# Optimization experiments

Measured on AMD Instinct MI355X. Metric: run time of the kernel, lower is better.

Reference implementation:

```python
import jax, jax.numpy as jnp
import numpy as np

D = 256          # input_dim (node embedding dim)
ATT_TIMES = 2
ATT_NUM = 2
DIN = D * ATT_NUM  # NTN input dim = 512
F = 16           # feature_map_dim


def setup_inputs() -> dict:
    key = jax.random.key(0)
    ks = jax.random.split(key, 10)
    x1 = jax.random.normal(ks[0], (120000, D), dtype=jnp.float32)
    x2 = jax.random.normal(ks[1], (100000, D), dtype=jnp.float32)
    # attention weight (glorot)
    W0 = jax.random.normal(ks[2], (D, D), dtype=jnp.float32) * (2.0 / (D + D)) ** 0.5
    # NTN params
    V = jax.random.normal(ks[3], (F, 2 * DIN), dtype=jnp.float32) * (2.0 / (F + 2 * DIN)) ** 0.5
    W = jax.random.normal(ks[4], (F, DIN, DIN), dtype=jnp.float32) * (2.0 / (DIN + DIN)) ** 0.5
    b = jax.random.normal(ks[5], (F,), dtype=jnp.float32)
    # projection MLP 16->8->4->2->1, torch Linear weights are (out, in)
    P0 = jax.random.normal(ks[6], (8, 16), dtype=jnp.float32) * (2.0 / (8 + 16)) ** 0.5
    P1 = jax.random.normal(ks[7], (4, 8), dtype=jnp.float32) * (2.0 / (4 + 8)) ** 0.5
    P2 = jax.random.normal(ks[8], (2, 4), dtype=jnp.float32) * (2.0 / (2 + 4)) ** 0.5
    P3 = jax.random.normal(ks[9], (1, 2), dtype=jnp.float32) * (2.0 / (1 + 2)) ** 0.5
    return {"x1": x1, "x2": x2, "W0": W0, "V": V, "W": W, "b": b,
            "P0": P0, "P1": P1, "P2": P2, "P3": P3}


def _attention(x, W0):
    # x: (N, D) -> (1, D*ATT_NUM) graph embedding.
    outs = []
    for _ in range(ATT_NUM):  # 'dot' style: same params each head (eye W), kept for faithfulness
        cur = x
        out = None
        for _ in range(ATT_TIMES):
            temp = jnp.mean(cur, axis=0, keepdims=True)          # (1, D)
            h_avg = jnp.tanh(temp @ W0)                          # att_weight=True
            att = jax.nn.sigmoid(cur @ h_avg.T)                  # (N, 1), W=eye in 'dot' style
            out = att.T @ cur                                    # (1, D)
            cur = cur * att
        outs.append(out)
    return jnp.concatenate(outs, axis=1)                         # (1, DIN)


def _ntn(g1, g2, V, W, b):
    # g1, g2: (1, DIN). Fused bilinear over all F feature maps.
    concat = jnp.concatenate([g1, g2], axis=1)                   # (1, 2*DIN)
    v_term = concat @ V.T                                        # (1, F)
    w_term = jnp.einsum('nd,fde,me->nf', g1, W, g2)              # (1, F)
    return jax.nn.sigmoid(v_term + w_term + b)                   # inneract = sigmoid


def reference(x1, x2, W0, V, W, b, P0, P1, P2, P3):
    g1 = _attention(x1, W0)
    g2 = _attention(x2, W0)
    x = _ntn(g1, g2, V, W, b)                                    # (1, F), branch 'an'
    for P in (P0, P1, P2, P3):                                   # Linear(no bias) + Sigmoid
        x = jax.nn.sigmoid(x @ P.T)
    return x                                                     # (1, 1)
```

## Files before the change

kernel.cpp:

```cpp
#include <hip/hip_runtime.h>
#include <math.h>

#define DD 256
#define REPS 8

#define OFF_SUMREP 0
#define OFF_H1P    4096
#define OFF_S1REP  4608
#define OFF_H2P    8704
#define OFF_OREP   9216
#define OFF_WTREP  13824
#define WS_FLOATS  13952
#define MIRROR_OFF_BYTES 65536

typedef float    f32x4 __attribute__((ext_vector_type(4)));
typedef float    f32x8 __attribute__((ext_vector_type(8)));
typedef _Float16 f16x4 __attribute__((ext_vector_type(4)));
typedef _Float16 f16x8 __attribute__((ext_vector_type(8)));

__device__ __forceinline__ float sigmoidf_(float x) { return 1.0f / (1.0f + __expf(-x)); }

__device__ __forceinline__ f32x8 ld8(const f16x8* p, size_t i) {
    return __builtin_convertvector(p[i], f32x8);
}
__device__ __forceinline__ f32x8 ld8(const f32x8* p, size_t i) { return p[i]; }

__device__ __forceinline__ float dot8(f32x8 a, f32x8 b) {
    f32x8 m = a * b;
    return ((m[0] + m[4]) + (m[1] + m[5])) + ((m[2] + m[6]) + (m[3] + m[7]));
}

__global__ void k_zero(float* __restrict__ ws) {
    int i = blockIdx.x * 256 + threadIdx.x;
    if (i < WS_FLOATS) ws[i] = 0.0f;
}

__device__ __forceinline__ void block_reduce_atomic4(f32x4 acc, int t, float* dst_base) {
    __shared__ f32x4 lds[256];
    lds[t] = acc;
    __syncthreads();
    if (t < 64) {
        f32x4 s = lds[t] + lds[t + 64] + lds[t + 128] + lds[t + 192];
        float* dst = dst_base + t * 4;
        atomicAdd(dst + 0, s.x); atomicAdd(dst + 1, s.y);
        atomicAdd(dst + 2, s.z); atomicAdd(dst + 3, s.w);
    }
}

__device__ __forceinline__ void block_reduce_atomic8(f32x8 acc, int t, float* dst_base) {
    __shared__ f32x8 lds8[256];
    lds8[t] = acc;
    __syncthreads();
    const float* lf = (const float*)lds8;
    float s = 0.f;
#pragma unroll
    for (int slot = 0; slot < 8; slot++) s += lf[slot * 256 + t];
    atomicAdd(dst_base + t, s);
}

template<bool WM>
__global__ void k_mean_t(const f32x4* __restrict__ x1, const f32x4* __restrict__ x2,
                         f16x4* __restrict__ m1, f16x4* __restrict__ m2,
                         int N1, int N2, float* __restrict__ ws) {
    int b = blockIdx.x, t = threadIdx.x;
    int inp = (b < 512) ? 0 : 1;
    int bl = inp ? (b - 512) : b;
    const f32x4* x = inp ? x2 : x1;
    f16x4* mm = inp ? m2 : m1;
    int N = inp ? N2 : N1;
    int col4 = t & 63, rg = t >> 6;
    f32x4 acc = {0.f, 0.f, 0.f, 0.f};
    for (int r = bl * 4 + rg; r < N; r += 2048) {
        size_t i0 = (size_t)r * 64 + col4;
        f32x4 v = x[i0];
        if (WM) mm[i0] = __builtin_convertvector(v, f16x4);
        acc += v;
    }
    block_reduce_atomic4(acc, t, ws + OFF_SUMREP + inp * (REPS * 256) + (bl & (REPS - 1)) * 256);
}

__global__ void k_hpart(const float* __restrict__ W0, float* __restrict__ ws,
                        int srcOff, int dstOff, int N1, int N2) {
    int inp = blockIdx.x >> 4, g = blockIdx.x & 15;
    int t = threadIdx.x;
    __shared__ float temp[16];
    if (t < 16) {
        const float* src = ws + srcOff + inp * (REPS * 256) + g * 16 + t;
        float s = 0.f;
#pragma unroll
        for (int r = 0; r < REPS; r++) s += src[r * 256];
        temp[t] = s * (1.0f / (float)(inp ? N2 : N1));
    }
    __syncthreads();
    float p = 0.f;
#pragma unroll
    for (int j = 0; j < 16; j++) p += temp[j] * W0[(g * 16 + j) * 256 + t];
    atomicAdd(ws + dstOff + inp * 256 + t, p);
}

template<typename T>
__global__ void k_att1_t(const T* __restrict__ b1, const T* __restrict__ b2,
                         int N1, int N2, float* __restrict__ ws) {
    int b = blockIdx.x, t = threadIdx.x;
    int inp = (b < 512) ? 0 : 1;
    int bl = inp ? (b - 512) : b;
    const T* x = inp ? b2 : b1;
    int N = inp ? N2 : N1;
    int lane = t & 63, w = t >> 6;
    int half = lane >> 5, l32 = lane & 31;
    f32x8 h1;
#pragma unroll
    for (int j = 0; j < 8; j++) h1[j] = tanhf(ws[OFF_H1P + inp * 256 + l32 * 8 + j]);
    f32x8 acc = {0.f, 0.f, 0.f, 0.f, 0.f, 0.f, 0.f, 0.f};
    int wid = bl * 4 + w;
    int base = wid * 2;
    for (; base + 1 < N; base += 4096) {
        int row = base + half;
        f32x8 v = ld8(x, (size_t)row * 32 + l32);
        float d = dot8(v, h1);
#pragma unroll
        for (int off = 16; off; off >>= 1) d += __shfl_xor(d, off, 64);
        acc += sigmoidf_(d) * v;
    }
    if (base < N && half == 0) {
        f32x8 v = ld8(x, (size_t)base * 32 + l32);
        float d = dot8(v, h1);
#pragma unroll
        for (int off = 16; off; off >>= 1) d += __shfl_xor(d, off, 64);
        acc += sigmoidf_(d) * v;
    }
    block_reduce_atomic8(acc, t, ws + OFF_S1REP + inp * (REPS * 256) + (bl & (REPS - 1)) * 256);
}

template<typename T>
__global__ void k_att2_t(const T* __restrict__ b1, const T* __restrict__ b2,
                         int N1, int N2, float* __restrict__ ws) {
    int b = blockIdx.x, t = threadIdx.x;
    int inp = (b < 512) ? 0 : 1;
    int bl = inp ? (b - 512) : b;
    const T* x = inp ? b2 : b1;
    int N = inp ? N2 : N1;
    int lane = t & 63, w = t >> 6;
    int half = lane >> 5, l32 = lane & 31;
    f32x8 h1, h2;
#pragma unroll
    for (int j = 0; j < 8; j++) {
        h1[j] = tanhf(ws[OFF_H1P + inp * 256 + l32 * 8 + j]);
        h2[j] = tanhf(ws[OFF_H2P + inp * 256 + l32 * 8 + j]);
    }
    f32x8 acc = {0.f, 0.f, 0.f, 0.f, 0.f, 0.f, 0.f, 0.f};
    int wid = bl * 4 + w;
    int base = wid * 2;
    for (; base + 1 < N; base += 4096) {
        int row = base + half;
        f32x8 v = ld8(x, (size_t)row * 32 + l32);
        float d = dot8(v, h1), e = dot8(v, h2);
#pragma unroll
        for (int off = 16; off; off >>= 1) {
            d += __shfl_xor(d, off, 64); e += __shfl_xor(e, off, 64);
        }
        float a1 = sigmoidf_(d);
        acc += (a1 * sigmoidf_(a1 * e)) * v;
    }
    if (base < N && half == 0) {
        f32x8 v = ld8(x, (size_t)base * 32 + l32);
        float d = dot8(v, h1), e = dot8(v, h2);
#pragma unroll
        for (int off = 16; off; off >>= 1) {
            d += __shfl_xor(d, off, 64); e += __shfl_xor(e, off, 64);
        }
        float a1 = sigmoidf_(d);
        acc += (a1 * sigmoidf_(a1 * e)) * v;
    }
    block_reduce_atomic8(acc, t, ws + OFF_OREP + inp * (REPS * 256) + (bl & (REPS - 1)) * 256);
}

__global__ void __launch_bounds__(256, 4)
k_ntn(const float* __restrict__ W, float* __restrict__ ws) {
    __shared__ __align__(16) float o_l[512];
    int b = blockIdx.x, t = threadIdx.x;
    {
        float s0 = 0.f, s1 = 0.f;
#pragma unroll
        for (int r2 = 0; r2 < REPS; r2++) {
            s0 += ws[OFF_OREP + r2 * 256 + t];
            s1 += ws[OFF_OREP + REPS * 256 + r2 * 256 + t];
        }
        o_l[t] = s0; o_l[256 + t] = s1;
    }
    __syncthreads();
    int lane = t & 63, w = t >> 6;
    f32x4 o2f = ((const f32x4*)(o_l + 256))[lane];
    int g = b * 4 + w;
    const f32x4* W4 = (const f32x4*)W;
    float wt[4];
    int fidx[4];
#pragma unroll
    for (int u = 0; u < 4; u++) {
        int row = g + u * 2048;
        const f32x4* q = W4 + (size_t)row * 128 + lane;
        f32x4 m = (q[0] + q[64]) * o2f;
        float p = (m.x + m.y) + (m.z + m.w);
#pragma unroll
        for (int off = 32; off; off >>= 1) p += __shfl_xor(p, off, 64);
        wt[u] = o_l[row & 255] * p;
        fidx[u] = row >> 9;
    }
    if (lane == 0) {
        float* dst = ws + OFF_WTREP + (b & (REPS - 1)) * 16;
#pragma unroll
        for (int u = 0; u < 4; u++) atomicAdd(dst + fidx[u], wt[u]);
    }
}

__global__ void k_final(const float* __restrict__ V, const float* __restrict__ bb,
                        const float* __restrict__ P0, const float* __restrict__ P1,
                        const float* __restrict__ P2, const float* __restrict__ P3,
                        float* __restrict__ ws, float* __restrict__ out) {
    int t = threadIdx.x;
    __shared__ float o_l[512];
    {
        float s0 = 0.f, s1 = 0.f;
#pragma unroll
        for (int r2 = 0; r2 < REPS; r2++) {
            s0 += ws[OFF_OREP + r2 * 256 + t];
            s1 += ws[OFF_OREP + REPS * 256 + r2 * 256 + t];
        }
        o_l[t] = s0; o_l[256 + t] = s1;
    }
    __syncthreads();
    int f = t >> 4, j = t & 15;
    float p = 0.f;
    for (int k = j; k < 1024; k += 16) {
        float cv = (k < 512) ? o_l[k & 255] : o_l[256 + (k & 255)];
        p += cv * V[f * 1024 + k];
    }
    __shared__ float red[256];
    __shared__ float sv[16];
    red[t] = p;
    __syncthreads();
    if (t < 16) {
        float v = 0.f;
#pragma unroll
        for (int q = 0; q < 16; q++) v += red[t * 16 + q];
        float wt = 0.f;
#pragma unroll
        for (int r = 0; r < REPS; r++) wt += ws[OFF_WTREP + r * 16 + t];
        sv[t] = sigmoidf_(v + wt + bb[t]);
    }
    __syncthreads();
    if (t == 0) {
        float y0[8], y1[4], y2[2];
#pragma unroll
        for (int i = 0; i < 8; i++) {
            float s = 0.f;
            for (int k = 0; k < 16; k++) s += P0[i * 16 + k] * sv[k];
            y0[i] = sigmoidf_(s);
        }
#pragma unroll
        for (int i = 0; i < 4; i++) {
            float s = 0.f;
            for (int k = 0; k < 8; k++) s += P1[i * 8 + k] * y0[k];
            y1[i] = sigmoidf_(s);
        }
#pragma unroll
        for (int i = 0; i < 2; i++) {
            float s = 0.f;
            for (int k = 0; k < 4; k++) s += P2[i * 4 + k] * y1[k];
            y2[i] = sigmoidf_(s);
        }
        out[0] = sigmoidf_(P3[0] * y2[0] + P3[1] * y2[1]);
    }
}

extern "C" void kernel_launch(void* const* d_in, const int* in_sizes, int n_in,
                              void* d_out, int out_size, void* d_ws, size_t ws_size,
                              hipStream_t stream) {
    const float* x1 = (const float*)d_in[0];
    const float* x2 = (const float*)d_in[1];
    const float* W0 = (const float*)d_in[2];
    const float* V  = (const float*)d_in[3];
    const float* W  = (const float*)d_in[4];
    const float* b  = (const float*)d_in[5];
    const float* P0 = (const float*)d_in[6];
    const float* P1 = (const float*)d_in[7];
    const float* P2 = (const float*)d_in[8];
    const float* P3 = (const float*)d_in[9];
    float* ws  = (float*)d_ws;
    float* out = (float*)d_out;
    int N1 = in_sizes[0] / DD;
    int N2 = in_sizes[1] / DD;

    const f32x4* x1v = (const f32x4*)x1;
    const f32x4* x2v = (const f32x4*)x2;
    f16x4* m1 = (f16x4*)((char*)d_ws + MIRROR_OFF_BYTES);
    f16x4* m2 = m1 + (size_t)N1 * 64;
    size_t need = (size_t)MIRROR_OFF_BYTES + ((size_t)N1 + N2) * DD * sizeof(_Float16);
    bool use_mirror = ws_size >= need;

    k_zero <<<55, 256, 0, stream>>>(ws);
    if (use_mirror) {
        k_mean_t<true>  <<<1024, 256, 0, stream>>>(x1v, x2v, m1, m2, N1, N2, ws);
        k_hpart         <<<32,   256, 0, stream>>>(W0, ws, OFF_SUMREP, OFF_H1P, N1, N2);
        k_att1_t<f16x8> <<<1024, 256, 0, stream>>>((const f16x8*)m1, (const f16x8*)m2, N1, N2, ws);
        k_hpart         <<<32,   256, 0, stream>>>(W0, ws, OFF_S1REP, OFF_H2P, N1, N2);
        k_att2_t<f16x8> <<<1024, 256, 0, stream>>>((const f16x8*)m1, (const f16x8*)m2, N1, N2, ws);
    } else {
        k_mean_t<false> <<<1024, 256, 0, stream>>>(x1v, x2v, nullptr, nullptr, N1, N2, ws);
        k_hpart         <<<32,   256, 0, stream>>>(W0, ws, OFF_SUMREP, OFF_H1P, N1, N2);
        k_att1_t<f32x8> <<<1024, 256, 0, stream>>>((const f32x8*)x1, (const f32x8*)x2, N1, N2, ws);
        k_hpart         <<<32,   256, 0, stream>>>(W0, ws, OFF_S1REP, OFF_H2P, N1, N2);
        k_att2_t<f32x8> <<<1024, 256, 0, stream>>>((const f32x8*)x1, (const f32x8*)x2, N1, N2, ws);
    }
    k_ntn  <<<512, 256, 0, stream>>>(W, ws);
    k_final<<<1,   256, 0, stream>>>(V, b, P0, P1, P2, P3, ws, out);
}
```

Baseline: 402.2 us.

## Drop fp16 mirror; stream fp32 inputs with wider grids and unrolled column sum

Removes the fp16 mirror copy of x1/x2 written during the mean pass. Both attention passes now read the original fp32 inputs directly, with the attention grids doubled to 2048 blocks. The column sum becomes a separate per-input kernel with four independent accumulators over a flat strided index. This drops the mirror write traffic but doubles the bytes each attention pass reads, so the net effect depends on whether the fp32 data stays in cache (the inputs total about 225 MB).

```diff
diff --git a/kernel.cpp b/kernel.cpp
--- a/kernel.cpp
+++ b/kernel.cpp
@@ -11,19 +11,11 @@
 #define OFF_OREP   9216
 #define OFF_WTREP  13824
 #define WS_FLOATS  13952
-#define MIRROR_OFF_BYTES 65536
 
 typedef float    f32x4 __attribute__((ext_vector_type(4)));
 typedef float    f32x8 __attribute__((ext_vector_type(8)));
-typedef _Float16 f16x4 __attribute__((ext_vector_type(4)));
-typedef _Float16 f16x8 __attribute__((ext_vector_type(8)));
 
 __device__ __forceinline__ float sigmoidf_(float x) { return 1.0f / (1.0f + __expf(-x)); }
-
-__device__ __forceinline__ f32x8 ld8(const f16x8* p, size_t i) {
-    return __builtin_convertvector(p[i], f32x8);
-}
-__device__ __forceinline__ f32x8 ld8(const f32x8* p, size_t i) { return p[i]; }
 
 __device__ __forceinline__ float dot8(f32x8 a, f32x8 b) {
     f32x8 m = a * b;
@@ -58,25 +50,23 @@
     atomicAdd(dst_base + t, s);
 }
 
-template<bool WM>
-__global__ void k_mean_t(const f32x4* __restrict__ x1, const f32x4* __restrict__ x2,
-                         f16x4* __restrict__ m1, f16x4* __restrict__ m2,
-                         int N1, int N2, float* __restrict__ ws) {
-    int b = blockIdx.x, t = threadIdx.x;
-    int inp = (b < 512) ? 0 : 1;
-    int bl = inp ? (b - 512) : b;
-    const f32x4* x = inp ? x2 : x1;
-    f16x4* mm = inp ? m2 : m1;
-    int N = inp ? N2 : N1;
-    int col4 = t & 63, rg = t >> 6;
-    f32x4 acc = {0.f, 0.f, 0.f, 0.f};
-    for (int r = bl * 4 + rg; r < N; r += 2048) {
-        size_t i0 = (size_t)r * 64 + col4;
-        f32x4 v = x[i0];
-        if (WM) mm[i0] = __builtin_convertvector(v, f16x4);
-        acc += v;
-    }
-    block_reduce_atomic4(acc, t, ws + OFF_SUMREP + inp * (REPS * 256) + (bl & (REPS - 1)) * 256);
+__global__ void k_colsum(const f32x4* __restrict__ x, int N, int inp,
+                         float* __restrict__ ws) {
+    int t = threadIdx.x;
+    const size_t STR = 1024 * 256;
+    size_t total = (size_t)N * 64;
+    size_t i = (size_t)blockIdx.x * 256 + t;
+    f32x4 a0 = {0.f,0.f,0.f,0.f}, a1 = a0, a2 = a0, a3 = a0;
+    for (; i + 3 * STR < total; i += 4 * STR) {
+        a0 += x[i];
+        a1 += x[i + STR];
+        a2 += x[i + 2 * STR];
+        a3 += x[i + 3 * STR];
+    }
+    for (; i < total; i += STR) a0 += x[i];
+    f32x4 acc = (a0 + a1) + (a2 + a3);
+    block_reduce_atomic4(acc, t,
+        ws + OFF_SUMREP + inp * (REPS * 256) + (blockIdx.x & (REPS - 1)) * 256);
 }
 
 __global__ void k_hpart(const float* __restrict__ W0, float* __restrict__ ws,
@@ -98,13 +88,12 @@
     atomicAdd(ws + dstOff + inp * 256 + t, p);
 }
 
-template<typename T>
-__global__ void k_att1_t(const T* __restrict__ b1, const T* __restrict__ b2,
-                         int N1, int N2, float* __restrict__ ws) {
+__global__ void k_att1(const f32x8* __restrict__ b1, const f32x8* __restrict__ b2,
+                       int N1, int N2, float* __restrict__ ws) {
     int b = blockIdx.x, t = threadIdx.x;
-    int inp = (b < 512) ? 0 : 1;
-    int bl = inp ? (b - 512) : b;
-    const T* x = inp ? b2 : b1;
+    int inp = (b < 1024) ? 0 : 1;
+    int bl = inp ? (b - 1024) : b;
+    const f32x8* x = inp ? b2 : b1;
     int N = inp ? N2 : N1;
     int lane = t & 63, w = t >> 6;
     int half = lane >> 5, l32 = lane & 31;
@@ -114,16 +103,16 @@
     f32x8 acc = {0.f, 0.f, 0.f, 0.f, 0.f, 0.f, 0.f, 0.f};
     int wid = bl * 4 + w;
     int base = wid * 2;
-    for (; base + 1 < N; base += 4096) {
+    for (; base + 1 < N; base += 8192) {
         int row = base + half;
-        f32x8 v = ld8(x, (size_t)row * 32 + l32);
+        f32x8 v = x[(size_t)row * 32 + l32];
         float d = dot8(v, h1);
 #pragma unroll
         for (int off = 16; off; off >>= 1) d += __shfl_xor(d, off, 64);
         acc += sigmoidf_(d) * v;
     }
     if (base < N && half == 0) {
-        f32x8 v = ld8(x, (size_t)base * 32 + l32);
+        f32x8 v = x[(size_t)base * 32 + l32];
         float d = dot8(v, h1);
 #pragma unroll
         for (int off = 16; off; off >>= 1) d += __shfl_xor(d, off, 64);
@@ -132,13 +121,12 @@
     block_reduce_atomic8(acc, t, ws + OFF_S1REP + inp * (REPS * 256) + (bl & (REPS - 1)) * 256);
 }
 
-template<typename T>
-__global__ void k_att2_t(const T* __restrict__ b1, const T* __restrict__ b2,
-                         int N1, int N2, float* __restrict__ ws) {
+__global__ void k_att2(const f32x8* __restrict__ b1, const f32x8* __restrict__ b2,
+                       int N1, int N2, float* __restrict__ ws) {
     int b = blockIdx.x, t = threadIdx.x;
-    int inp = (b < 512) ? 0 : 1;
-    int bl = inp ? (b - 512) : b;
-    const T* x = inp ? b2 : b1;
+    int inp = (b < 1024) ? 0 : 1;
+    int bl = inp ? (b - 1024) : b;
+    const f32x8* x = inp ? b2 : b1;
     int N = inp ? N2 : N1;
     int lane = t & 63, w = t >> 6;
     int half = lane >> 5, l32 = lane & 31;
@@ -151,9 +139,9 @@
     f32x8 acc = {0.f, 0.f, 0.f, 0.f, 0.f, 0.f, 0.f, 0.f};
     int wid = bl * 4 + w;
     int base = wid * 2;
-    for (; base + 1 < N; base += 4096) {
+    for (; base + 1 < N; base += 8192) {
         int row = base + half;
-        f32x8 v = ld8(x, (size_t)row * 32 + l32);
+        f32x8 v = x[(size_t)row * 32 + l32];
         float d = dot8(v, h1), e = dot8(v, h2);
 #pragma unroll
         for (int off = 16; off; off >>= 1) {
@@ -163,7 +151,7 @@
         acc += (a1 * sigmoidf_(a1 * e)) * v;
     }
     if (base < N && half == 0) {
-        f32x8 v = ld8(x, (size_t)base * 32 + l32);
+        f32x8 v = x[(size_t)base * 32 + l32];
         float d = dot8(v, h1), e = dot8(v, h2);
 #pragma unroll
         for (int off = 16; off; off >>= 1) {
@@ -291,27 +279,13 @@
     int N1 = in_sizes[0] / DD;
     int N2 = in_sizes[1] / DD;
 
-    const f32x4* x1v = (const f32x4*)x1;
-    const f32x4* x2v = (const f32x4*)x2;
-    f16x4* m1 = (f16x4*)((char*)d_ws + MIRROR_OFF_BYTES);
-    f16x4* m2 = m1 + (size_t)N1 * 64;
-    size_t need = (size_t)MIRROR_OFF_BYTES + ((size_t)N1 + N2) * DD * sizeof(_Float16);
-    bool use_mirror = ws_size >= need;
-
-    k_zero <<<55, 256, 0, stream>>>(ws);
-    if (use_mirror) {
-        k_mean_t<true>  <<<1024, 256, 0, stream>>>(x1v, x2v, m1, m2, N1, N2, ws);
-        k_hpart         <<<32,   256, 0, stream>>>(W0, ws, OFF_SUMREP, OFF_H1P, N1, N2);
-        k_att1_t<f16x8> <<<1024, 256, 0, stream>>>((const f16x8*)m1, (const f16x8*)m2, N1, N2, ws);
-        k_hpart         <<<32,   256, 0, stream>>>(W0, ws, OFF_S1REP, OFF_H2P, N1, N2);
-        k_att2_t<f16x8> <<<1024, 256, 0, stream>>>((const f16x8*)m1, (const f16x8*)m2, N1, N2, ws);
-    } else {
-        k_mean_t<false> <<<1024, 256, 0, stream>>>(x1v, x2v, nullptr, nullptr, N1, N2, ws);
-        k_hpart         <<<32,   256, 0, stream>>>(W0, ws, OFF_SUMREP, OFF_H1P, N1, N2);
-        k_att1_t<f32x8> <<<1024, 256, 0, stream>>>((const f32x8*)x1, (const f32x8*)x2, N1, N2, ws);
-        k_hpart         <<<32,   256, 0, stream>>>(W0, ws, OFF_S1REP, OFF_H2P, N1, N2);
-        k_att2_t<f32x8> <<<1024, 256, 0, stream>>>((const f32x8*)x1, (const f32x8*)x2, N1, N2, ws);
-    }
-    k_ntn  <<<512, 256, 0, stream>>>(W, ws);
-    k_final<<<1,   256, 0, stream>>>(V, b, P0, P1, P2, P3, ws, out);
-}
+    k_zero  <<<55,   256, 0, stream>>>(ws);
+    k_colsum<<<1024, 256, 0, stream>>>((const f32x4*)x1, N1, 0, ws);
+    k_colsum<<<1024, 256, 0, stream>>>((const f32x4*)x2, N2, 1, ws);
+    k_hpart <<<32,   256, 0, stream>>>(W0, ws, OFF_SUMREP, OFF_H1P, N1, N2);
+    k_att1  <<<2048, 256, 0, stream>>>((const f32x8*)x1, (const f32x8*)x2, N1, N2, ws);
+    k_hpart <<<32,   256, 0, stream>>>(W0, ws, OFF_S1REP, OFF_H2P, N1, N2);
+    k_att2  <<<2048, 256, 0, stream>>>((const f32x8*)x1, (const f32x8*)x2, N1, N2, ws);
+    k_ntn   <<<512,  256, 0, stream>>>(W, ws);
+    k_final <<<1,    256, 0, stream>>>(V, b, P0, P1, P2, P3, ws, out);
+}
```

New measurement: 440.0 us. 9.4% more time.
